# Kernel tuning notes

Measured on AMD Instinct MI355X. Metric: run time of the kernel, lower is better.

Reference implementation:

```python
import jax, jax.numpy as jnp
import numpy as np

N_NODES = 100000
N_EDGES = 1000000
NEG_SLOPE = 0.2


def gat_conv(x, src, dst, W, al, ar, b, res, activation):
    """DGL-style GATConv. res is None (no residual), 'id' (identity residual), or a [in,H*D] matrix."""
    H, D = al.shape
    n = x.shape[0]
    feat = (x @ W).reshape(n, H, D)                      # [N,H,D]
    el = jnp.einsum('nhd,hd->nh', feat, al)              # [N,H]
    er = jnp.einsum('nhd,hd->nh', feat, ar)              # [N,H]
    e = jax.nn.leaky_relu(el[src] + er[dst], NEG_SLOPE)  # [E,H]
    # edge softmax over incoming edges of each dst node
    m = jax.lax.stop_gradient(jax.ops.segment_max(e, dst, num_segments=n))
    ex = jnp.exp(e - m[dst])
    s = jax.ops.segment_sum(ex, dst, num_segments=n)
    alpha = ex / s[dst]                                  # [E,H]
    out = jax.ops.segment_sum(feat[src] * alpha[:, :, None], dst, num_segments=n)  # [N,H,D]
    if res == 'id':
        out = out + x.reshape(n, H, D)
    elif res is not None:
        out = out + (x @ res).reshape(n, H, D)
    out = out + b.reshape(1, H, D)
    if activation is not None:
        out = activation(out)
    return out


def setup_inputs() -> dict:
    key = jax.random.key(0)
    ks = jax.random.split(key, 20)
    F_IN, HID = 128, 32
    H1, H2, H3 = 4, 4, 1
    C = 40
    sc = 0.1
    inp = {
        'x':   jax.random.normal(ks[0], (N_NODES, F_IN), dtype=jnp.float32),
        'src': jax.random.randint(ks[1], (N_EDGES,), 0, N_NODES, dtype=jnp.int32),
        'dst': jax.random.randint(ks[2], (N_EDGES,), 0, N_NODES, dtype=jnp.int32),
        # layer 1: in=128 -> H1*HID=128, no residual, elu
        'W1':  sc * jax.random.normal(ks[3], (F_IN, H1 * HID), dtype=jnp.float32),
        'al1': sc * jax.random.normal(ks[4], (H1, HID), dtype=jnp.float32),
        'ar1': sc * jax.random.normal(ks[5], (H1, HID), dtype=jnp.float32),
        'b1':  jnp.zeros((H1 * HID,), dtype=jnp.float32),
        # layer 2: in=128 -> H2*HID=128, identity residual, elu
        'W2':  sc * jax.random.normal(ks[6], (H1 * HID, H2 * HID), dtype=jnp.float32),
        'al2': sc * jax.random.normal(ks[7], (H2, HID), dtype=jnp.float32),
        'ar2': sc * jax.random.normal(ks[8], (H2, HID), dtype=jnp.float32),
        'b2':  jnp.zeros((H2 * HID,), dtype=jnp.float32),
        # layer 3 (output): in=128 -> H3*HID=32, projected residual, no activation
        'W3':  sc * jax.random.normal(ks[9], (H2 * HID, H3 * HID), dtype=jnp.float32),
        'al3': sc * jax.random.normal(ks[10], (H3, HID), dtype=jnp.float32),
        'ar3': sc * jax.random.normal(ks[11], (H3, HID), dtype=jnp.float32),
        'b3':  jnp.zeros((H3 * HID,), dtype=jnp.float32),
        'res3': sc * jax.random.normal(ks[12], (H2 * HID, H3 * HID), dtype=jnp.float32),
        # final classifier
        'Wfc': sc * jax.random.normal(ks[13], (HID, C), dtype=jnp.float32),
        'bfc': jnp.zeros((C,), dtype=jnp.float32),
    }
    return inp


def reference(x, src, dst, W1, al1, ar1, b1, W2, al2, ar2, b2, W3, al3, ar3, b3, res3, Wfc, bfc):
    n = x.shape[0]
    h = gat_conv(x, src, dst, W1, al1, ar1, b1, None, jax.nn.elu).reshape(n, -1)   # [N, 128]
    h = gat_conv(h, src, dst, W2, al2, ar2, b2, 'id', jax.nn.elu).reshape(n, -1)   # [N, 128]
    h = gat_conv(h, src, dst, W3, al3, ar3, b3, res3, None).mean(axis=1)           # [N, 32]
    return h @ Wfc + bfc                                                           # [N, 40]
```

## Files before the change

### kernel.cpp

```cpp
#include <hip/hip_runtime.h>
#include <cstdint>
#include <cstddef>

#define NN 100000
#define NE 1000000
#define GEMM_BLOCKS 1563
#define TICKET_BLOCKS 3907
#define CAST_BLOCKS 12500
#define LOG2E 1.4426950408896340736f

typedef unsigned int uint;
typedef unsigned short ushort;
typedef __attribute__((ext_vector_type(8))) short bfrag;
typedef __attribute__((ext_vector_type(4))) float f32x4;

__device__ __forceinline__ ushort f2bf(float f){
  uint u = __float_as_uint(f);
  u += 0x7fffu + ((u >> 16) & 1u);
  return (ushort)(u >> 16);
}
__device__ __forceinline__ float bflo(uint p){ return __uint_as_float(p << 16); }
__device__ __forceinline__ float bfhi(uint p){ return __uint_as_float(p & 0xffff0000u); }


__global__ __launch_bounds__(256) void k_scan_local(const int* __restrict__ cnt4, int* __restrict__ shoff,
                                                    int* __restrict__ rowptr, int* __restrict__ bsum){
  __shared__ int sm[256];
  int t = threadIdx.x;
  int i = blockIdx.x*256 + t;
  int v = 0;
  if (i < NN){
    int4 c = ((const int4*)cnt4)[i];
    v = c.x + c.y + c.z + c.w;
    int4 so;
    so.x = 0; so.y = c.x; so.z = c.x + c.y; so.w = c.x + c.y + c.z;
    ((int4*)shoff)[i] = so;
  }
  sm[t] = v;
  __syncthreads();
  for (int off=1; off<256; off<<=1){
    int u = (t>=off) ? sm[t-off] : 0;
    __syncthreads();
    sm[t] += u;
    __syncthreads();
  }
  if (i < NN) rowptr[i] = sm[t] - v;
  if (t == 255) bsum[blockIdx.x] = sm[255];
}

__global__ __launch_bounds__(512) void k_scan_bsum(const int* __restrict__ bsum, int* __restrict__ boff, int nb){
  __shared__ int sm[512];
  int t = threadIdx.x;
  int v = (t < nb) ? bsum[t] : 0;
  sm[t] = v;
  __syncthreads();
  for (int off=1; off<512; off<<=1){
    int u = (t>=off) ? sm[t-off] : 0;
    __syncthreads();
    sm[t] += u;
    __syncthreads();
  }
  if (t < nb) boff[t] = sm[t] - v;
}

__global__ __launch_bounds__(256) void k_scan_add(int* __restrict__ rowptr, const int* __restrict__ boff){
  int i = blockIdx.x*256 + threadIdx.x;
  if (i < NN) rowptr[i] += boff[i>>8];
  else if (i == NN) rowptr[NN] = NE;
}


__global__ __launch_bounds__(256) void k_dhist(const int* __restrict__ rowptr, int* __restrict__ dbin){
  __shared__ int lh[256];
  int t = threadIdx.x;
  lh[t] = 0;
  __syncthreads();
  int n = blockIdx.x*256 + t;
  if (n < NN){
    int deg = rowptr[n+1] - rowptr[n];
    atomicAdd(&lh[deg > 255 ? 255 : deg], 1);
  }
  __syncthreads();
  if (lh[t] > 0) atomicAdd(&dbin[t], lh[t]);
}

__global__ __launch_bounds__(256) void k_dscan(int* __restrict__ dbin){
  __shared__ int sm[256];
  int t = threadIdx.x;
  int v = dbin[t];
  sm[t] = v;
  __syncthreads();
  for (int off=1; off<256; off<<=1){
    int u = (t>=off) ? sm[t-off] : 0;
    __syncthreads();
    sm[t] += u;
    __syncthreads();
  }
  dbin[t] = sm[t] - v;
}

__global__ __launch_bounds__(256) void k_dscat(const int* __restrict__ rowptr, int* __restrict__ dbin,
                                               int* __restrict__ perm){
  __shared__ int lh[256];
  __shared__ int lbase[256];
  int t = threadIdx.x;
  lh[t] = 0;
  __syncthreads();
  int n = blockIdx.x*256 + t;
  int bin = -1, lticket = 0;
  if (n < NN){
    int deg = rowptr[n+1] - rowptr[n];
    bin = deg > 255 ? 255 : deg;
    lticket = atomicAdd(&lh[bin], 1);
  }
  __syncthreads();
  if (lh[t] > 0) lbase[t] = atomicAdd(&dbin[t], lh[t]);
  __syncthreads();
  if (n < NN) perm[lbase[bin] + lticket] = n;
}


__device__ __forceinline__ void bfrag_body(const float* __restrict__ B1, const float* __restrict__ B2,
                                           int n1, int n2, int NT, ushort* __restrict__ out, int i){
  if (i >= NT*4*64) return;
  int l = i & 63, ks = (i>>6)&3, nt = i>>8;
  int col = nt*16 + (l&15);
  int k0  = ks*32 + (l>>4)*8;
  const float* B; int stride, c;
  if (col < n1){ B = B1; stride = n1; c = col; }
  else         { B = B2; stride = n2; c = col - n1; }
  ushort v[8];
  #pragma unroll
  for (int j=0;j<8;j++) v[j] = f2bf(B[(size_t)(k0+j)*stride + c]);
  uint4 pk;
  pk.x = (uint)v[0] | ((uint)v[1]<<16);
  pk.y = (uint)v[2] | ((uint)v[3]<<16);
  pk.z = (uint)v[4] | ((uint)v[5]<<16);
  pk.w = (uint)v[6] | ((uint)v[7]<<16);
  *(uint4*)(out + (size_t)i*8) = pk;
}

__global__ __launch_bounds__(256) void k_prep(const float* __restrict__ x, ushort* __restrict__ xb,
                                              const float* __restrict__ W1, const float* __restrict__ W2,
                                              const float* __restrict__ W3, const float* __restrict__ res3,
                                              ushort* __restrict__ Bf1, ushort* __restrict__ Bf2,
                                              ushort* __restrict__ Bf3,
                                              const int* __restrict__ dst, int* __restrict__ cnt4,
                                              int* __restrict__ tick){
  int bid = blockIdx.x, t = threadIdx.x;
  if (bid < CAST_BLOCKS){
    int i = bid*256 + t;
    float4 v = ((const float4*)x)[i];
    uint2 p;
    p.x = (uint)f2bf(v.x) | ((uint)f2bf(v.y)<<16);
    p.y = (uint)f2bf(v.z) | ((uint)f2bf(v.w)<<16);
    ((uint2*)xb)[i] = p;
  } else if (bid < CAST_BLOCKS + 20){
    int r = bid - CAST_BLOCKS;
    if (r < 8)       bfrag_body(W1, nullptr, 128, 0, 8, Bf1, r*256 + t);
    else if (r < 16) bfrag_body(W2, nullptr, 128, 0, 8, Bf2, (r-8)*256 + t);
    else             bfrag_body(W3, res3,    32, 32, 4, Bf3, (r-16)*256 + t);
  } else {
    int e = (bid - CAST_BLOCKS - 20)*256 + t;
    if (e < NE) tick[e] = atomicAdd(&cnt4[(uint)dst[e]*4u + (e & 3)], 1);
  }
}


template<int NT, int NTF, int H>
__device__ __forceinline__ void gemm_body(int bid, const ushort* __restrict__ Ab, const ushort* __restrict__ Bf,
                                          ushort* __restrict__ featb, float* __restrict__ Cres,
                                          const float* __restrict__ al, const float* __restrict__ ar,
                                          float* __restrict__ el, float* __restrict__ er, int M){
  __shared__ ushort Bs[NT*2048];
  int t = threadIdx.x;
  #pragma unroll
  for (int i=0; i<NT; ++i)
    ((uint4*)Bs)[i*256 + t] = ((const uint4*)Bf)[i*256 + t];
  __syncthreads();

  int l = t & 63, w = t >> 6;
  int rw = bid*64 + w*16;
  int c = l & 15, g = l >> 4;

  f32x4 acc[NT];
  #pragma unroll
  for (int nt=0;nt<NT;nt++) acc[nt] = (f32x4){0.f,0.f,0.f,0.f};

  int rowA = rw + c; if (rowA >= M) rowA = M-1;
  const ushort* Ap = Ab + (size_t)rowA*128 + g*8;
  const bfrag* Bp = (const bfrag*)Bs;

  #pragma unroll
  for (int ks=0; ks<4; ++ks){
    bfrag a = *(const bfrag*)(Ap + ks*32);
    #pragma unroll
    for (int nt=0; nt<NT; ++nt){
      bfrag b = Bp[(nt*4+ks)*64 + l];
      acc[nt] = __builtin_amdgcn_mfma_f32_16x16x32_bf16(a, b, acc[nt], 0, 0, 0);
    }
  }

  float alv[H][2], arv[H][2];
  #pragma unroll
  for (int h=0;h<H;h++){
    alv[h][0]=al[h*32+c]*LOG2E;    arv[h][0]=ar[h*32+c]*LOG2E;
    alv[h][1]=al[h*32+16+c]*LOG2E; arv[h][1]=ar[h*32+16+c]*LOG2E;
  }

  #pragma unroll
  for (int reg=0; reg<4; ++reg){
    int row = rw + g*4 + reg;
    bool ok = row < M;
    #pragma unroll
    for (int h=0;h<H;h++){
      float pl = acc[2*h][reg]*alv[h][0] + acc[2*h+1][reg]*alv[h][1];
      float pr = acc[2*h][reg]*arv[h][0] + acc[2*h+1][reg]*arv[h][1];
      #pragma unroll
      for (int off=1; off<16; off<<=1){ pl += __shfl_xor(pl,off); pr += __shfl_xor(pr,off); }
      if (ok && c==0){ el[(size_t)row*H + h] = pl; er[(size_t)row*H + h] = pr; }
    }
    if (ok){
      #pragma unroll
      for (int nt=0; nt<NTF; ++nt)
        featb[(size_t)row*(NTF*16) + nt*16 + c] = f2bf(acc[nt][reg]);
      #pragma unroll
      for (int nt=NTF; nt<NT; ++nt)
        Cres[(size_t)row*((NT-NTF)*16) + (nt-NTF)*16 + c] = acc[nt][reg];
    }
  }
}

template<int NT, int NTF, int H>
__global__ __launch_bounds__(256) void k_gemm_mfma(const ushort* __restrict__ Ab, const ushort* __restrict__ Bf,
                                                   ushort* __restrict__ featb, float* __restrict__ Cres,
                                                   const float* __restrict__ al, const float* __restrict__ ar,
                                                   float* __restrict__ el, float* __restrict__ er, int M){
  gemm_body<NT,NTF,H>(blockIdx.x, Ab, Bf, featb, Cres, al, ar, el, er, M);
}

__global__ __launch_bounds__(256) void k_gemm1_place(const ushort* __restrict__ xb, const ushort* __restrict__ Bf1,
                                                     ushort* __restrict__ featb,
                                                     const float* __restrict__ al, const float* __restrict__ ar,
                                                     float* __restrict__ el, float* __restrict__ er,
                                                     const int* __restrict__ src, const int* __restrict__ dst,
                                                     const int* __restrict__ rowptr, const int* __restrict__ shoff,
                                                     const int* __restrict__ tick, int* __restrict__ csr){
  int bid = blockIdx.x;
  if (bid < GEMM_BLOCKS){
    gemm_body<8,8,4>(bid, xb, Bf1, featb, nullptr, al, ar, el, er, NN);
  } else {
    int e = (bid - GEMM_BLOCKS)*256 + threadIdx.x;
    if (e < NE){
      int d = dst[e];
      csr[rowptr[d] + shoff[(uint)d*4u + (e & 3)] + tick[e]] = src[e];
    }
  }
}


template<int RK>
__global__ __launch_bounds__(256) void k_agg4(const int* __restrict__ rowptr, const int* __restrict__ csr,
                                              const int* __restrict__ perm,
                                              const ushort* __restrict__ feat,
                                              const float* __restrict__ el, const float* __restrict__ er,
                                              const void* __restrict__ res, const float* __restrict__ bias,
                                              ushort* __restrict__ out, int act){
  int t = threadIdx.x;
  int l15 = t & 15;
  int node = perm[blockIdx.x*16 + (t>>4)];

  int beg = rowptr[node], deg = rowptr[node+1] - beg;
  int hm = l15 >> 2;
  float erh = er[(size_t)node*4 + hm];
  const int* cp = csr + beg;
  uint fo = (uint)l15*8u;

  float ssum = 0.f;
  float a0=0.f,a1=0.f,a2=0.f,a3=0.f,a4=0.f,a5=0.f,a6=0.f,a7=0.f;

  int ei = 0;
  for (; ei+4 <= deg; ei += 4){
    int s0 = cp[ei], s1 = cp[ei+1], s2 = cp[ei+2], s3 = cp[ei+3];
    uint4 p0 = *(const uint4*)(feat + ((uint)s0*128u + fo));
    uint4 p1 = *(const uint4*)(feat + ((uint)s1*128u + fo));
    uint4 p2 = *(const uint4*)(feat + ((uint)s2*128u + fo));
    uint4 p3 = *(const uint4*)(feat + ((uint)s3*128u + fo));
    float v0 = el[(uint)s0*4u + hm] + erh; v0 = fmaxf(v0, 0.2f*v0);
    float v1 = el[(uint)s1*4u + hm] + erh; v1 = fmaxf(v1, 0.2f*v1);
    float v2 = el[(uint)s2*4u + hm] + erh; v2 = fmaxf(v2, 0.2f*v2);
    float v3 = el[(uint)s3*4u + hm] + erh; v3 = fmaxf(v3, 0.2f*v3);
    float w0 = __builtin_amdgcn_exp2f(v0);
    float w1 = __builtin_amdgcn_exp2f(v1);
    float w2 = __builtin_amdgcn_exp2f(v2);
    float w3 = __builtin_amdgcn_exp2f(v3);
    ssum += (w0 + w1) + (w2 + w3);
    a0 += w0*bflo(p0.x) + w1*bflo(p1.x) + w2*bflo(p2.x) + w3*bflo(p3.x);
    a1 += w0*bfhi(p0.x) + w1*bfhi(p1.x) + w2*bfhi(p2.x) + w3*bfhi(p3.x);
    a2 += w0*bflo(p0.y) + w1*bflo(p1.y) + w2*bflo(p2.y) + w3*bflo(p3.y);
    a3 += w0*bfhi(p0.y) + w1*bfhi(p1.y) + w2*bfhi(p2.y) + w3*bfhi(p3.y);
    a4 += w0*bflo(p0.z) + w1*bflo(p1.z) + w2*bflo(p2.z) + w3*bflo(p3.z);
    a5 += w0*bfhi(p0.z) + w1*bfhi(p1.z) + w2*bfhi(p2.z) + w3*bfhi(p3.z);
    a6 += w0*bflo(p0.w) + w1*bflo(p1.w) + w2*bflo(p2.w) + w3*bflo(p3.w);
    a7 += w0*bfhi(p0.w) + w1*bfhi(p1.w) + w2*bfhi(p2.w) + w3*bfhi(p3.w);
  }
  for (; ei < deg; ++ei){
    int s0 = cp[ei];
    uint4 p0 = *(const uint4*)(feat + ((uint)s0*128u + fo));
    float v0 = el[(uint)s0*4u + hm] + erh; v0 = fmaxf(v0, 0.2f*v0);
    float w0 = __builtin_amdgcn_exp2f(v0);
    ssum += w0;
    a0 += w0*bflo(p0.x); a1 += w0*bfhi(p0.x);
    a2 += w0*bflo(p0.y); a3 += w0*bfhi(p0.y);
    a4 += w0*bflo(p0.z); a5 += w0*bfhi(p0.z);
    a6 += w0*bflo(p0.w); a7 += w0*bfhi(p0.w);
  }

  float inv = (deg > 0) ? 1.f/ssum : 0.f;
  float o0=a0*inv, o1=a1*inv, o2=a2*inv, o3=a3*inv;
  float o4=a4*inv, o5=a5*inv, o6=a6*inv, o7=a7*inv;
  if (RK == 1){
    uint4 rv = *(const uint4*)((const ushort*)res + (size_t)node*128 + fo);
    o0 += bflo(rv.x); o1 += bfhi(rv.x); o2 += bflo(rv.y); o3 += bfhi(rv.y);
    o4 += bflo(rv.z); o5 += bfhi(rv.z); o6 += bflo(rv.w); o7 += bfhi(rv.w);
  }
  float4 bv0 = *(const float4*)(bias + l15*8);
  float4 bv1 = *(const float4*)(bias + l15*8 + 4);
  o0 += bv0.x; o1 += bv0.y; o2 += bv0.z; o3 += bv0.w;
  o4 += bv1.x; o5 += bv1.y; o6 += bv1.z; o7 += bv1.w;
  if (act){
    o0 = (o0>0.f)?o0:__expf(o0)-1.f;
    o1 = (o1>0.f)?o1:__expf(o1)-1.f;
    o2 = (o2>0.f)?o2:__expf(o2)-1.f;
    o3 = (o3>0.f)?o3:__expf(o3)-1.f;
    o4 = (o4>0.f)?o4:__expf(o4)-1.f;
    o5 = (o5>0.f)?o5:__expf(o5)-1.f;
    o6 = (o6>0.f)?o6:__expf(o6)-1.f;
    o7 = (o7>0.f)?o7:__expf(o7)-1.f;
  }
  uint4 pk;
  pk.x = (uint)f2bf(o0) | ((uint)f2bf(o1)<<16);
  pk.y = (uint)f2bf(o2) | ((uint)f2bf(o3)<<16);
  pk.z = (uint)f2bf(o4) | ((uint)f2bf(o5)<<16);
  pk.w = (uint)f2bf(o6) | ((uint)f2bf(o7)<<16);
  *(uint4*)(out + (size_t)node*128 + fo) = pk;
}


__global__ __launch_bounds__(256) void k_agg1(const int* __restrict__ rowptr, const int* __restrict__ csr,
                                              const int* __restrict__ perm,
                                              const ushort* __restrict__ feat,
                                              const float* __restrict__ el, const float* __restrict__ er,
                                              const float* __restrict__ res, const float* __restrict__ bias,
                                              float* __restrict__ h3){
  int t = threadIdx.x;
  int l7 = t & 7;
  int node = perm[blockIdx.x*32 + (t>>3)];

  int beg = rowptr[node], deg = rowptr[node+1] - beg;
  float er0 = er[node];
  const int* cp = csr + beg;
  uint fo = (uint)l7*4u;

  float ssum = 0.f, a0=0.f, a1=0.f, a2=0.f, a3=0.f;
  int ei = 0;
  for (; ei+2 <= deg; ei += 2){
    int s0 = cp[ei], s1 = cp[ei+1];
    uint2 p0 = *(const uint2*)(feat + ((uint)s0*32u + fo));
    uint2 p1 = *(const uint2*)(feat + ((uint)s1*32u + fo));
    float v0 = el[s0] + er0; v0 = fmaxf(v0, 0.2f*v0);
    float v1 = el[s1] + er0; v1 = fmaxf(v1, 0.2f*v1);
    float w0 = __builtin_amdgcn_exp2f(v0);
    float w1 = __builtin_amdgcn_exp2f(v1);
    ssum += w0 + w1;
    a0 += w0*bflo(p0.x) + w1*bflo(p1.x);
    a1 += w0*bfhi(p0.x) + w1*bfhi(p1.x);
    a2 += w0*bflo(p0.y) + w1*bflo(p1.y);
    a3 += w0*bfhi(p0.y) + w1*bfhi(p1.y);
  }
  if (ei < deg){
    int s0 = cp[ei];
    uint2 p0 = *(const uint2*)(feat + ((uint)s0*32u + fo));
    float v0 = el[s0] + er0; v0 = fmaxf(v0, 0.2f*v0);
    float w0 = __builtin_amdgcn_exp2f(v0);
    ssum += w0;
    a0 += w0*bflo(p0.x); a1 += w0*bfhi(p0.x);
    a2 += w0*bflo(p0.y); a3 += w0*bfhi(p0.y);
  }

  float inv = (deg > 0) ? 1.f/ssum : 0.f;
  float4 rv = *(const float4*)(res + (size_t)node*32 + fo);
  float4 bv = *(const float4*)(bias + fo);
  float4 ov;
  ov.x = a0*inv + rv.x + bv.x;
  ov.y = a1*inv + rv.y + bv.y;
  ov.z = a2*inv + rv.z + bv.z;
  ov.w = a3*inv + rv.w + bv.w;
  *(float4*)(h3 + (size_t)node*32 + fo) = ov;
}


__global__ __launch_bounds__(256) void k_fc(const float* __restrict__ h, const float* __restrict__ W,
                                            const float* __restrict__ b, float* __restrict__ out){
  __shared__ float Ws[32*40];
  __shared__ float Hs[64][33];
  __shared__ float bs[40];
  int t = threadIdx.x;
  for (int i=t; i<1280; i+=256) Ws[i] = W[i];
  if (t < 40) bs[t] = b[t];
  int n0 = blockIdx.x*64;
  for (int idx=t; idx<512; idx+=256){
    int r = idx>>3, c4 = idx&7;
    float4 v;
    if (n0 + r < NN) v = *(const float4*)(h + (size_t)(n0+r)*32 + c4*4);
    else v = make_float4(0.f,0.f,0.f,0.f);
    Hs[r][c4*4+0]=v.x; Hs[r][c4*4+1]=v.y; Hs[r][c4*4+2]=v.z; Hs[r][c4*4+3]=v.w;
  }
  __syncthreads();
  int n = t>>2, cg = t&3;
  float acc[10];
  #pragma unroll
  for (int j=0;j<10;j++) acc[j] = 0.f;
  #pragma unroll
  for (int k=0;k<32;k++){
    float hv = Hs[n][k];
    #pragma unroll
    for (int j=0;j<10;j++) acc[j] += hv * Ws[k*40 + cg + 4*j];
  }
  int row = n0 + n;
  if (row < NN){
    #pragma unroll
    for (int j=0;j<10;j++) out[(size_t)row*40 + cg + 4*j] = acc[j] + bs[cg+4*j];
  }
}


extern "C" void kernel_launch(void* const* d_in, const int* in_sizes, int n_in,
                              void* d_out, int out_size, void* d_ws, size_t ws_size,
                              hipStream_t stream){
  const float* x    = (const float*)d_in[0];
  const int*   src  = (const int*)  d_in[1];
  const int*   dst  = (const int*)  d_in[2];
  const float* W1   = (const float*)d_in[3];
  const float* al1  = (const float*)d_in[4];
  const float* ar1  = (const float*)d_in[5];
  const float* b1   = (const float*)d_in[6];
  const float* W2   = (const float*)d_in[7];
  const float* al2  = (const float*)d_in[8];
  const float* ar2  = (const float*)d_in[9];
  const float* b2   = (const float*)d_in[10];
  const float* W3   = (const float*)d_in[11];
  const float* al3  = (const float*)d_in[12];
  const float* ar3  = (const float*)d_in[13];
  const float* b3   = (const float*)d_in[14];
  const float* res3 = (const float*)d_in[15];
  const float* Wfc  = (const float*)d_in[16];
  const float* bfc  = (const float*)d_in[17];
  float* out = (float*)d_out;

  char* ws = (char*)d_ws;
  size_t o = 0;
  auto alloc = [&](size_t bytes)->char*{
    char* p = ws + o;
    o += (bytes + 255) & ~(size_t)255;
    return p;
  };
  int*    rowptr = (int*)   alloc((size_t)(NN+1)*4);
  int*    cnt4   = (int*)   alloc((size_t)NN*4*4);
  int*    shoff  = (int*)   alloc((size_t)NN*4*4);
  int*    bsum   = (int*)   alloc(512*4);
  int*    boff   = (int*)   alloc(512*4);
  int*    dbin   = (int*)   alloc(256*4);
  int*    perm   = (int*)   alloc((size_t)NN*4);
  int*    tick   = (int*)   alloc((size_t)NE*4);
  int*    csr    = (int*)   alloc((size_t)NE*4);
  float*  el     = (float*) alloc((size_t)NN*4*4);
  float*  er     = (float*) alloc((size_t)NN*4*4);
  ushort* xb     = (ushort*)alloc((size_t)NN*128*2);
  ushort* featb  = (ushort*)alloc((size_t)NN*128*2);
  ushort* h1b    = (ushort*)alloc((size_t)NN*128*2);
  ushort* h2b    = (ushort*)alloc((size_t)NN*128*2);
  float*  res3p  = (float*) alloc((size_t)NN*32*4);
  float*  h3     = (float*) alloc((size_t)NN*32*4);
  ushort* Bf1    = (ushort*)alloc((size_t)8*4*64*8*2);
  ushort* Bf2    = (ushort*)alloc((size_t)8*4*64*8*2);
  ushort* Bf3    = (ushort*)alloc((size_t)4*4*64*8*2);
  (void)ws_size; (void)n_in; (void)in_sizes; (void)out_size;

  hipMemsetAsync(cnt4, 0, (size_t)NN*4*4, stream);
  hipMemsetAsync(dbin, 0, 256*4, stream);
  k_prep<<<CAST_BLOCKS+20+TICKET_BLOCKS, 256, 0, stream>>>(x, xb, W1, W2, W3, res3,
                                                           Bf1, Bf2, Bf3, dst, cnt4, tick);
  int nb = (NN+255)/256;
  k_scan_local<<<nb, 256, 0, stream>>>(cnt4, shoff, rowptr, bsum);
  k_scan_bsum<<<1, 512, 0, stream>>>(bsum, boff, nb);
  k_scan_add<<<(NN+1+255)/256, 256, 0, stream>>>(rowptr, boff);

  k_dhist<<<nb, 256, 0, stream>>>(rowptr, dbin);
  k_dscan<<<1, 256, 0, stream>>>(dbin);
  k_dscat<<<nb, 256, 0, stream>>>(rowptr, dbin, perm);

  k_gemm1_place<<<GEMM_BLOCKS+TICKET_BLOCKS, 256, 0, stream>>>(xb, Bf1, featb, al1, ar1, el, er,
                                                               src, dst, rowptr, shoff, tick, csr);
  k_agg4<0><<<NN/16, 256, 0, stream>>>(rowptr, csr, perm, featb, el, er, nullptr, b1, h1b, 1);

  k_gemm_mfma<8,8,4><<<GEMM_BLOCKS, 256, 0, stream>>>(h1b, Bf2, featb, nullptr, al2, ar2, el, er, NN);
  k_agg4<1><<<NN/16, 256, 0, stream>>>(rowptr, csr, perm, featb, el, er, h1b, b2, h2b, 1);

  k_gemm_mfma<4,2,1><<<GEMM_BLOCKS, 256, 0, stream>>>(h2b, Bf3, featb, res3p, al3, ar3, el, er, NN);
  k_agg1<<<NN/32, 256, 0, stream>>>(rowptr, csr, perm, featb, el, er, res3p, b3, h3);
  k_fc<<<GEMM_BLOCKS, 256, 0, stream>>>(h3, Wfc, bfc, out);
}
```

Measured before the change: 301.8 us.

## Fuse x bf16 cast into layer-1 GEMM and merge scan/histogram launches

Layer-1 GEMM now reads fp32 x directly and converts it to bf16 in registers, which removes the separate cast pass and the xb buffer. The ticket atomics now share a launch with the GEMM, CSR placement is fused with the degree histogram, and the block-sum scan is merged with the add pass. This cuts kernel launches and roughly 25MB of intermediate traffic. In exchange the GEMM reads A straight from global memory with no LDS staging for B, so it may run less efficiently per block.

```diff
diff --git a/kernel.cpp b/kernel.cpp
--- a/kernel.cpp
+++ b/kernel.cpp
@@ -6,7 +6,7 @@
 #define NE 1000000
 #define GEMM_BLOCKS 1563
 #define TICKET_BLOCKS 3907
-#define CAST_BLOCKS 12500
+#define NB_SCAN 391
 #define LOG2E 1.4426950408896340736f
 
 typedef unsigned int uint;
@@ -21,103 +21,6 @@
 }
 __device__ __forceinline__ float bflo(uint p){ return __uint_as_float(p << 16); }
 __device__ __forceinline__ float bfhi(uint p){ return __uint_as_float(p & 0xffff0000u); }
-
-
-__global__ __launch_bounds__(256) void k_scan_local(const int* __restrict__ cnt4, int* __restrict__ shoff,
-                                                    int* __restrict__ rowptr, int* __restrict__ bsum){
-  __shared__ int sm[256];
-  int t = threadIdx.x;
-  int i = blockIdx.x*256 + t;
-  int v = 0;
-  if (i < NN){
-    int4 c = ((const int4*)cnt4)[i];
-    v = c.x + c.y + c.z + c.w;
-    int4 so;
-    so.x = 0; so.y = c.x; so.z = c.x + c.y; so.w = c.x + c.y + c.z;
-    ((int4*)shoff)[i] = so;
-  }
-  sm[t] = v;
-  __syncthreads();
-  for (int off=1; off<256; off<<=1){
-    int u = (t>=off) ? sm[t-off] : 0;
-    __syncthreads();
-    sm[t] += u;
-    __syncthreads();
-  }
-  if (i < NN) rowptr[i] = sm[t] - v;
-  if (t == 255) bsum[blockIdx.x] = sm[255];
-}
-
-__global__ __launch_bounds__(512) void k_scan_bsum(const int* __restrict__ bsum, int* __restrict__ boff, int nb){
-  __shared__ int sm[512];
-  int t = threadIdx.x;
-  int v = (t < nb) ? bsum[t] : 0;
-  sm[t] = v;
-  __syncthreads();
-  for (int off=1; off<512; off<<=1){
-    int u = (t>=off) ? sm[t-off] : 0;
-    __syncthreads();
-    sm[t] += u;
-    __syncthreads();
-  }
-  if (t < nb) boff[t] = sm[t] - v;
-}
-
-__global__ __launch_bounds__(256) void k_scan_add(int* __restrict__ rowptr, const int* __restrict__ boff){
-  int i = blockIdx.x*256 + threadIdx.x;
-  if (i < NN) rowptr[i] += boff[i>>8];
-  else if (i == NN) rowptr[NN] = NE;
-}
-
-
-__global__ __launch_bounds__(256) void k_dhist(const int* __restrict__ rowptr, int* __restrict__ dbin){
-  __shared__ int lh[256];
-  int t = threadIdx.x;
-  lh[t] = 0;
-  __syncthreads();
-  int n = blockIdx.x*256 + t;
-  if (n < NN){
-    int deg = rowptr[n+1] - rowptr[n];
-    atomicAdd(&lh[deg > 255 ? 255 : deg], 1);
-  }
-  __syncthreads();
-  if (lh[t] > 0) atomicAdd(&dbin[t], lh[t]);
-}
-
-__global__ __launch_bounds__(256) void k_dscan(int* __restrict__ dbin){
-  __shared__ int sm[256];
-  int t = threadIdx.x;
-  int v = dbin[t];
-  sm[t] = v;
-  __syncthreads();
-  for (int off=1; off<256; off<<=1){
-    int u = (t>=off) ? sm[t-off] : 0;
-    __syncthreads();
-    sm[t] += u;
-    __syncthreads();
-  }
-  dbin[t] = sm[t] - v;
-}
-
-__global__ __launch_bounds__(256) void k_dscat(const int* __restrict__ rowptr, int* __restrict__ dbin,
-                                               int* __restrict__ perm){
-  __shared__ int lh[256];
-  __shared__ int lbase[256];
-  int t = threadIdx.x;
-  lh[t] = 0;
-  __syncthreads();
-  int n = blockIdx.x*256 + t;
-  int bin = -1, lticket = 0;
-  if (n < NN){
-    int deg = rowptr[n+1] - rowptr[n];
-    bin = deg > 255 ? 255 : deg;
-    lticket = atomicAdd(&lh[bin], 1);
-  }
-  __syncthreads();
-  if (lh[t] > 0) lbase[t] = atomicAdd(&dbin[t], lh[t]);
-  __syncthreads();
-  if (n < NN) perm[lbase[bin] + lticket] = n;
-}
 
 
 __device__ __forceinline__ void bfrag_body(const float* __restrict__ B1, const float* __restrict__ B2,
@@ -140,30 +43,188 @@
   *(uint4*)(out + (size_t)i*8) = pk;
 }
 
-__global__ __launch_bounds__(256) void k_prep(const float* __restrict__ x, ushort* __restrict__ xb,
-                                              const float* __restrict__ W1, const float* __restrict__ W2,
-                                              const float* __restrict__ W3, const float* __restrict__ res3,
-                                              ushort* __restrict__ Bf1, ushort* __restrict__ Bf2,
-                                              ushort* __restrict__ Bf3,
-                                              const int* __restrict__ dst, int* __restrict__ cnt4,
-                                              int* __restrict__ tick){
+__global__ __launch_bounds__(256) void k_packs(const float* __restrict__ W1, const float* __restrict__ W2,
+                                               const float* __restrict__ W3, const float* __restrict__ res3,
+                                               ushort* __restrict__ Bf1, ushort* __restrict__ Bf2,
+                                               ushort* __restrict__ Bf3){
+  int r = blockIdx.x, t = threadIdx.x;
+  if (r < 8)       bfrag_body(W1, nullptr, 128, 0, 8, Bf1, r*256 + t);
+  else if (r < 16) bfrag_body(W2, nullptr, 128, 0, 8, Bf2, (r-8)*256 + t);
+  else             bfrag_body(W3, res3,    32, 32, 4, Bf3, (r-16)*256 + t);
+}
+
+
+__global__ __launch_bounds__(256, 4)
+void k_gemm1_ticket(const float* __restrict__ x, const ushort* __restrict__ Bf1,
+                    ushort* __restrict__ featb,
+                    const float* __restrict__ al, const float* __restrict__ ar,
+                    float* __restrict__ el, float* __restrict__ er,
+                    const int* __restrict__ dst, int* __restrict__ cnt4, int* __restrict__ tick){
   int bid = blockIdx.x, t = threadIdx.x;
-  if (bid < CAST_BLOCKS){
-    int i = bid*256 + t;
-    float4 v = ((const float4*)x)[i];
-    uint2 p;
-    p.x = (uint)f2bf(v.x) | ((uint)f2bf(v.y)<<16);
-    p.y = (uint)f2bf(v.z) | ((uint)f2bf(v.w)<<16);
-    ((uint2*)xb)[i] = p;
-  } else if (bid < CAST_BLOCKS + 20){
-    int r = bid - CAST_BLOCKS;
-    if (r < 8)       bfrag_body(W1, nullptr, 128, 0, 8, Bf1, r*256 + t);
-    else if (r < 16) bfrag_body(W2, nullptr, 128, 0, 8, Bf2, (r-8)*256 + t);
-    else             bfrag_body(W3, res3,    32, 32, 4, Bf3, (r-16)*256 + t);
+  if (bid >= GEMM_BLOCKS){
+    int e = (bid - GEMM_BLOCKS)*256 + t;
+    if (e < NE) tick[e] = atomicAdd(&cnt4[(uint)dst[e]*4u + (e & 3)], 1);
+    return;
+  }
+
+  int l = t & 63, w = t >> 6;
+  int rw = bid*64 + w*16;
+  int c = l & 15, g = l >> 4;
+
+  f32x4 acc[8];
+  #pragma unroll
+  for (int nt=0;nt<8;nt++) acc[nt] = (f32x4){0.f,0.f,0.f,0.f};
+
+  int rowA = rw + c; if (rowA >= NN) rowA = NN-1;
+  const float* Ap = x + (size_t)rowA*128 + g*8;
+  const bfrag* Bp = (const bfrag*)Bf1;
+
+  #pragma unroll
+  for (int ks=0; ks<4; ++ks){
+    float4 f0 = *(const float4*)(Ap + ks*32);
+    float4 f1 = *(const float4*)(Ap + ks*32 + 4);
+    bfrag a;
+    a[0]=(short)f2bf(f0.x); a[1]=(short)f2bf(f0.y); a[2]=(short)f2bf(f0.z); a[3]=(short)f2bf(f0.w);
+    a[4]=(short)f2bf(f1.x); a[5]=(short)f2bf(f1.y); a[6]=(short)f2bf(f1.z); a[7]=(short)f2bf(f1.w);
+    #pragma unroll
+    for (int nt=0; nt<8; ++nt){
+      bfrag b = Bp[(nt*4+ks)*64 + l];
+      acc[nt] = __builtin_amdgcn_mfma_f32_16x16x32_bf16(a, b, acc[nt], 0, 0, 0);
+    }
+  }
+
+  float alv[4][2], arv[4][2];
+  #pragma unroll
+  for (int h=0;h<4;h++){
+    alv[h][0]=al[h*32+c]*LOG2E;    arv[h][0]=ar[h*32+c]*LOG2E;
+    alv[h][1]=al[h*32+16+c]*LOG2E; arv[h][1]=ar[h*32+16+c]*LOG2E;
+  }
+
+  #pragma unroll
+  for (int reg=0; reg<4; ++reg){
+    int row = rw + g*4 + reg;
+    bool ok = row < NN;
+    #pragma unroll
+    for (int h=0;h<4;h++){
+      float pl = acc[2*h][reg]*alv[h][0] + acc[2*h+1][reg]*alv[h][1];
+      float pr = acc[2*h][reg]*arv[h][0] + acc[2*h+1][reg]*arv[h][1];
+      #pragma unroll
+      for (int off=1; off<16; off<<=1){ pl += __shfl_xor(pl,off); pr += __shfl_xor(pr,off); }
+      if (ok && c==0){ el[(size_t)row*4 + h] = pl; er[(size_t)row*4 + h] = pr; }
+    }
+    if (ok){
+      #pragma unroll
+      for (int nt=0; nt<8; ++nt)
+        featb[(size_t)row*128 + nt*16 + c] = f2bf(acc[nt][reg]);
+    }
+  }
+}
+
+
+__global__ __launch_bounds__(256) void k_scan_local(const int* __restrict__ cnt4, int* __restrict__ shoff,
+                                                    int* __restrict__ rowptr, int* __restrict__ bsum){
+  __shared__ int sm[256];
+  int t = threadIdx.x;
+  int i = blockIdx.x*256 + t;
+  int v = 0;
+  if (i < NN){
+    int4 cc = ((const int4*)cnt4)[i];
+    v = cc.x + cc.y + cc.z + cc.w;
+    int4 so;
+    so.x = 0; so.y = cc.x; so.z = cc.x + cc.y; so.w = cc.x + cc.y + cc.z;
+    ((int4*)shoff)[i] = so;
+  }
+  sm[t] = v;
+  __syncthreads();
+  for (int off=1; off<256; off<<=1){
+    int u = (t>=off) ? sm[t-off] : 0;
+    __syncthreads();
+    sm[t] += u;
+    __syncthreads();
+  }
+  if (i < NN) rowptr[i] = sm[t] - v;
+  if (t == 255) bsum[blockIdx.x] = sm[255];
+}
+
+__global__ __launch_bounds__(512) void k_scan_finish(int* __restrict__ rowptr, const int* __restrict__ bsum){
+  __shared__ int sm[512];
+  __shared__ int ex[512];
+  int t = threadIdx.x;
+  int v = (t < NB_SCAN) ? bsum[t] : 0;
+  sm[t] = v;
+  __syncthreads();
+  for (int off=1; off<512; off<<=1){
+    int u = (t>=off) ? sm[t-off] : 0;
+    __syncthreads();
+    sm[t] += u;
+    __syncthreads();
+  }
+  ex[t] = sm[t] - v;
+  __syncthreads();
+  int i = blockIdx.x*512 + t;
+  if (i < NN) rowptr[i] += ex[i>>8];
+  else if (i == NN) rowptr[NN] = NE;
+}
+
+
+__global__ __launch_bounds__(256) void k_place_dhist(const int* __restrict__ src, const int* __restrict__ dst,
+                                                     const int* __restrict__ rowptr, const int* __restrict__ shoff,
+                                                     const int* __restrict__ tick, int* __restrict__ csr,
+                                                     int* __restrict__ dbin){
+  __shared__ int lh[256];
+  int bid = blockIdx.x, t = threadIdx.x;
+  if (bid < TICKET_BLOCKS){
+    int e = bid*256 + t;
+    if (e < NE){
+      int d = dst[e];
+      csr[rowptr[d] + shoff[(uint)d*4u + (e & 3)] + tick[e]] = src[e];
+    }
   } else {
-    int e = (bid - CAST_BLOCKS - 20)*256 + t;
-    if (e < NE) tick[e] = atomicAdd(&cnt4[(uint)dst[e]*4u + (e & 3)], 1);
-  }
+    lh[t] = 0;
+    __syncthreads();
+    int n = (bid - TICKET_BLOCKS)*256 + t;
+    if (n < NN){
+      int deg = rowptr[n+1] - rowptr[n];
+      atomicAdd(&lh[deg > 255 ? 255 : deg], 1);
+    }
+    __syncthreads();
+    if (lh[t] > 0) atomicAdd(&dbin[t], lh[t]);
+  }
+}
+
+__global__ __launch_bounds__(256) void k_dscan(int* __restrict__ dbin){
+  __shared__ int sm[256];
+  int t = threadIdx.x;
+  int v = dbin[t];
+  sm[t] = v;
+  __syncthreads();
+  for (int off=1; off<256; off<<=1){
+    int u = (t>=off) ? sm[t-off] : 0;
+    __syncthreads();
+    sm[t] += u;
+    __syncthreads();
+  }
+  dbin[t] = sm[t] - v;
+}
+
+__global__ __launch_bounds__(256) void k_dscat(const int* __restrict__ rowptr, int* __restrict__ dbin,
+                                               int* __restrict__ perm){
+  __shared__ int lh[256];
+  __shared__ int lbase[256];
+  int t = threadIdx.x;
+  lh[t] = 0;
+  __syncthreads();
+  int n = blockIdx.x*256 + t;
+  int bin = -1, lticket = 0;
+  if (n < NN){
+    int deg = rowptr[n+1] - rowptr[n];
+    bin = deg > 255 ? 255 : deg;
+    lticket = atomicAdd(&lh[bin], 1);
+  }
+  __syncthreads();
+  if (lh[t] > 0) lbase[t] = atomicAdd(&dbin[t], lh[t]);
+  __syncthreads();
+  if (n < NN) perm[lbase[bin] + lticket] = n;
 }
 
 
@@ -237,25 +298,6 @@
                                                    const float* __restrict__ al, const float* __restrict__ ar,
                                                    float* __restrict__ el, float* __restrict__ er, int M){
   gemm_body<NT,NTF,H>(blockIdx.x, Ab, Bf, featb, Cres, al, ar, el, er, M);
-}
-
-__global__ __launch_bounds__(256) void k_gemm1_place(const ushort* __restrict__ xb, const ushort* __restrict__ Bf1,
-                                                     ushort* __restrict__ featb,
-                                                     const float* __restrict__ al, const float* __restrict__ ar,
-                                                     float* __restrict__ el, float* __restrict__ er,
-                                                     const int* __restrict__ src, const int* __restrict__ dst,
-                                                     const int* __restrict__ rowptr, const int* __restrict__ shoff,
-                                                     const int* __restrict__ tick, int* __restrict__ csr){
-  int bid = blockIdx.x;
-  if (bid < GEMM_BLOCKS){
-    gemm_body<8,8,4>(bid, xb, Bf1, featb, nullptr, al, ar, el, er, NN);
-  } else {
-    int e = (bid - GEMM_BLOCKS)*256 + threadIdx.x;
-    if (e < NE){
-      int d = dst[e];
-      csr[rowptr[d] + shoff[(uint)d*4u + (e & 3)] + tick[e]] = src[e];
-    }
-  }
 }
 
 
@@ -469,14 +511,12 @@
   int*    cnt4   = (int*)   alloc((size_t)NN*4*4);
   int*    shoff  = (int*)   alloc((size_t)NN*4*4);
   int*    bsum   = (int*)   alloc(512*4);
-  int*    boff   = (int*)   alloc(512*4);
   int*    dbin   = (int*)   alloc(256*4);
   int*    perm   = (int*)   alloc((size_t)NN*4);
   int*    tick   = (int*)   alloc((size_t)NE*4);
   int*    csr    = (int*)   alloc((size_t)NE*4);
   float*  el     = (float*) alloc((size_t)NN*4*4);
   float*  er     = (float*) alloc((size_t)NN*4*4);
-  ushort* xb     = (ushort*)alloc((size_t)NN*128*2);
   ushort* featb  = (ushort*)alloc((size_t)NN*128*2);
   ushort* h1b    = (ushort*)alloc((size_t)NN*128*2);
   ushort* h2b    = (ushort*)alloc((size_t)NN*128*2);
@@ -489,19 +529,19 @@
 
   hipMemsetAsync(cnt4, 0, (size_t)NN*4*4, stream);
   hipMemsetAsync(dbin, 0, 256*4, stream);
-  k_prep<<<CAST_BLOCKS+20+TICKET_BLOCKS, 256, 0, stream>>>(x, xb, W1, W2, W3, res3,
-                                                           Bf1, Bf2, Bf3, dst, cnt4, tick);
-  int nb = (NN+255)/256;
-  k_scan_local<<<nb, 256, 0, stream>>>(cnt4, shoff, rowptr, bsum);
-  k_scan_bsum<<<1, 512, 0, stream>>>(bsum, boff, nb);
-  k_scan_add<<<(NN+1+255)/256, 256, 0, stream>>>(rowptr, boff);
-
-  k_dhist<<<nb, 256, 0, stream>>>(rowptr, dbin);
+
+  k_packs<<<20, 256, 0, stream>>>(W1, W2, W3, res3, Bf1, Bf2, Bf3);
+
+  k_gemm1_ticket<<<GEMM_BLOCKS+TICKET_BLOCKS, 256, 0, stream>>>(x, Bf1, featb, al1, ar1, el, er,
+                                                                dst, cnt4, tick);
+
+  k_scan_local<<<NB_SCAN, 256, 0, stream>>>(cnt4, shoff, rowptr, bsum);
+  k_scan_finish<<<(NN+1+511)/512, 512, 0, stream>>>(rowptr, bsum);
+
+  k_place_dhist<<<TICKET_BLOCKS+NB_SCAN, 256, 0, stream>>>(src, dst, rowptr, shoff, tick, csr, dbin);
   k_dscan<<<1, 256, 0, stream>>>(dbin);
-  k_dscat<<<nb, 256, 0, stream>>>(rowptr, dbin, perm);
-
-  k_gemm1_place<<<GEMM_BLOCKS+TICKET_BLOCKS, 256, 0, stream>>>(xb, Bf1, featb, al1, ar1, el, er,
-                                                               src, dst, rowptr, shoff, tick, csr);
+  k_dscat<<<NB_SCAN, 256, 0, stream>>>(rowptr, dbin, perm);
+
   k_agg4<0><<<NN/16, 256, 0, stream>>>(rowptr, csr, perm, featb, el, er, nullptr, b1, h1b, 1);
 
   k_gemm_mfma<8,8,4><<<GEMM_BLOCKS, 256, 0, stream>>>(h1b, Bf2, featb, nullptr, al2, ar2, el, er, NN);
```

After: 295.7 us. -2.0%, faster.
